# Performance work log

Measured on AMD Instinct MI355X. Metric: run time of the kernel, lower is better.

The kernel has to match this reference:

```python
import jax, jax.numpy as jnp
import numpy as np

B, L, H, U = 4, 4096, 1024, 1024


def setup_inputs() -> dict:
    key = jax.random.key(0)
    k0, k1, k2, k3 = jax.random.split(key, 4)
    inputs = jax.random.normal(k0, (B, L, H), dtype=jnp.float32)
    # linear layer params (torch default init scale ~ 1/sqrt(fan_in))
    W_rkv = jax.random.normal(k1, (H, 3 * U), dtype=jnp.float32) / np.sqrt(H)
    b_rkv = jnp.zeros((3 * U,), dtype=jnp.float32)
    W_o = jax.random.normal(k2, (U, H), dtype=jnp.float32) / np.sqrt(U)
    b_o = jnp.zeros((H,), dtype=jnp.float32)
    # nu_log init exactly as in the torch module
    r_min, r_max = 0.9, 0.999
    u = jax.random.uniform(k3, (U,), dtype=jnp.float32)
    nu_log = jnp.log(-0.5 * jnp.log(u * (r_max ** 2 - r_min ** 2) + r_min ** 2))
    gamma_log = jnp.zeros((U,), dtype=jnp.float32)
    return {"inputs": inputs, "W_rkv": W_rkv, "b_rkv": b_rkv,
            "W_o": W_o, "b_o": b_o, "nu_log": nu_log, "gamma_log": gamma_log}


def reference(inputs, W_rkv, b_rkv, W_o, b_o, nu_log, gamma_log):
    # projections
    rkv = jnp.einsum('blh,hu->blu', inputs, W_rkv) + b_rkv  # [B,L,3U]
    r, k, v = jnp.split(rkv, 3, axis=-1)
    r = jax.nn.sigmoid(r)
    k = jnp.exp(k)
    kv = k * v
    u = jnp.concatenate([kv, k], axis=-1)                   # [B,L,2U]
    nu = jnp.exp(jnp.concatenate([nu_log, nu_log]))         # [2U]
    gamma = jnp.exp(nu_log + gamma_log) - 1.0               # [U]
    lam = jnp.exp(-nu)                                      # per-channel decay
    # The torch log-depth doubling scan computes the linear recurrence
    # y_t = lam * y_{t-1} + u_t (y_0 = u_0). Use an associative scan over L.
    a = jnp.broadcast_to(lam, u.shape)

    def combine(c1, c2):
        a1, x1 = c1
        a2, x2 = c2
        return (a1 * a2, x1 * a2 + x2)

    _, y = jax.lax.associative_scan(combine, (a, u), axis=1)  # [B,L,2U]
    u1, u2 = jnp.split(y, 2, axis=-1)
    x = (u1 + gamma * kv) / (u2 + gamma * k + 1e-6) * r       # [B,L,U]
    return jnp.einsum('blu,uh->blh', x, W_o) + b_o
```

## Files before the change

### kernel.cpp

```cpp
#include <hip/hip_runtime.h>
#include <hip/hip_bf16.h>
#include <cstdint>
#include <cstddef>

constexpr int NB = 4;
constexpr int NL = 4096;
constexpr int NH = 1024;
constexpr int NU = 1024;
constexpr int NM = NB * NL;
constexpr int NCHUNK = 32;
constexpr int CLEN = NL / NCHUNK;

typedef __bf16 bf16x8 __attribute__((ext_vector_type(8)));
typedef __bf16 bf16x4 __attribute__((ext_vector_type(4)));
typedef float  f32x4  __attribute__((ext_vector_type(4)));

__global__ __launch_bounds__(256) void cast_f32_to_bf16(
    const float* __restrict__ in, __bf16* __restrict__ out, int n4) {
  int stride = gridDim.x * 256;
  for (int i = blockIdx.x * 256 + threadIdx.x; i < n4; i += stride) {
    const float4 v = reinterpret_cast<const float4*>(in)[i];
    bf16x4 o;
    o[0] = (__bf16)v.x; o[1] = (__bf16)v.y; o[2] = (__bf16)v.z; o[3] = (__bf16)v.w;
    reinterpret_cast<bf16x4*>(out)[i] = o;
  }
}

__global__ __launch_bounds__(256) void transpose_cast(
    const float* __restrict__ W, __bf16* __restrict__ Wt, int K, int N) {
  __shared__ float tile[32][33];
  int tx = threadIdx.x, ty = threadIdx.y;
  int n0 = blockIdx.x * 32, k0 = blockIdx.y * 32;
  #pragma unroll
  for (int i = 0; i < 32; i += 8)
    tile[ty + i][tx] = W[(size_t)(k0 + ty + i) * N + n0 + tx];
  __syncthreads();
  #pragma unroll
  for (int i = 0; i < 32; i += 8)
    Wt[(size_t)(n0 + ty + i) * K + k0 + tx] = (__bf16)tile[tx][ty + i];
}

constexpr int GBM = 128, GBN = 128, GBK = 64;

template<int EPI>
__global__ __launch_bounds__(256) void gemm_bf16(
    const __bf16* __restrict__ A, const __bf16* __restrict__ Bt,
    int M, int N, int K,
    const float* __restrict__ bias,
    float* __restrict__ out_r, float* __restrict__ out_k, float* __restrict__ out_v,
    float* __restrict__ out_f32) {
  __shared__ __attribute__((aligned(16))) __bf16 lA[GBM * GBK];
  __shared__ __attribute__((aligned(16))) __bf16 lB[GBN * GBK];

  const int tid = threadIdx.x;
  const int lane = tid & 63;
  const int w = tid >> 6;
  const int ntn = N / GBN;
  const int nwg = gridDim.x;
  const int bid = blockIdx.x;
  const int cpx = nwg >> 3;
  const int swz = (bid & 7) * cpx + (bid >> 3);
  const int mt = swz / ntn, nt = swz % ntn;
  const size_t m0 = (size_t)mt * GBM;
  const size_t n0 = (size_t)nt * GBN;

  const int wm = w >> 1, wn = w & 1;

  f32x4 acc[4][4];
  #pragma unroll
  for (int i = 0; i < 4; ++i)
    #pragma unroll
    for (int j = 0; j < 4; ++j) acc[i][j] = (f32x4)0.f;

  const int KT = K / GBK;
  for (int kt = 0; kt < KT; ++kt) {
    #pragma unroll
    for (int i = 0; i < 4; ++i) {
      int chunk = w * 4 + i;
      int off = chunk * 1024 + lane * 16;
      int row = off >> 7;
      int colb = off & 127;
      const __bf16* ga = A + (m0 + row) * K + kt * GBK + (colb >> 1);
      __builtin_amdgcn_global_load_lds(
          (const __attribute__((address_space(1))) unsigned int*)ga,
          (__attribute__((address_space(3))) unsigned int*)((char*)lA + chunk * 1024),
          16, 0, 0);
      const __bf16* gb = Bt + (n0 + row) * K + kt * GBK + (colb >> 1);
      __builtin_amdgcn_global_load_lds(
          (const __attribute__((address_space(1))) unsigned int*)gb,
          (__attribute__((address_space(3))) unsigned int*)((char*)lB + chunk * 1024),
          16, 0, 0);
    }
    __syncthreads();
    #pragma unroll
    for (int kk = 0; kk < GBK; kk += 32) {
      bf16x8 av[4], bv[4];
      #pragma unroll
      for (int f = 0; f < 4; ++f)
        av[f] = *(const bf16x8*)&lA[(wm * 64 + f * 16 + (lane & 15)) * GBK + kk + (lane >> 4) * 8];
      #pragma unroll
      for (int f = 0; f < 4; ++f)
        bv[f] = *(const bf16x8*)&lB[(wn * 64 + f * 16 + (lane & 15)) * GBK + kk + (lane >> 4) * 8];
      #pragma unroll
      for (int i = 0; i < 4; ++i)
        #pragma unroll
        for (int j = 0; j < 4; ++j)
          acc[i][j] = __builtin_amdgcn_mfma_f32_16x16x32_bf16(av[i], bv[j], acc[i][j], 0, 0, 0);
    }
    __syncthreads();
  }

  #pragma unroll
  for (int i = 0; i < 4; ++i) {
    #pragma unroll
    for (int j = 0; j < 4; ++j) {
      #pragma unroll
      for (int r = 0; r < 4; ++r) {
        int row = (int)m0 + wm * 64 + i * 16 + (lane >> 4) * 4 + r;
        int col = (int)n0 + wn * 64 + j * 16 + (lane & 15);
        float val = acc[i][j][r] + bias[col];
        if constexpr (EPI == 0) {
          int reg = col >> 10;
          int u = col & 1023;
          size_t idx = (size_t)row * NU + u;
          if (reg == 0)      out_r[idx] = 1.f / (1.f + __expf(-val));
          else if (reg == 1) out_k[idx] = __expf(val);
          else               out_v[idx] = val;
        } else {
          out_f32[(size_t)row * N + col] = val;
        }
      }
    }
  }
}

__global__ __launch_bounds__(256) void scan_pass1(
    const float* __restrict__ kbuf, const float* __restrict__ vbuf,
    const float* __restrict__ nu_log,
    float* __restrict__ S1, float* __restrict__ S2) {
  int u = blockIdx.x * 256 + threadIdx.x;
  int c = blockIdx.y;
  int b = blockIdx.z;
  float lam = __expf(-__expf(nu_log[u]));
  size_t base = ((size_t)b * NL + (size_t)c * CLEN) * NU + u;
  float y1 = 0.f, y2 = 0.f;
  #pragma unroll 4
  for (int t = 0; t < CLEN; ++t) {
    float kk = kbuf[base + (size_t)t * NU];
    float vv = vbuf[base + (size_t)t * NU];
    y1 = fmaf(lam, y1, kk * vv);
    y2 = fmaf(lam, y2, kk);
  }
  size_t si = ((size_t)b * NCHUNK + c) * NU + u;
  S1[si] = y1;
  S2[si] = y2;
}

__global__ __launch_bounds__(256) void scan_combine(
    const float* __restrict__ S1, const float* __restrict__ S2,
    const float* __restrict__ nu_log,
    float* __restrict__ C1, float* __restrict__ C2) {
  int u = blockIdx.x * 256 + threadIdx.x;
  int b = blockIdx.y;
  float lamCL = __expf(-__expf(nu_log[u]) * (float)CLEN);
  float y1 = 0.f, y2 = 0.f;
  for (int c = 0; c < NCHUNK; ++c) {
    size_t si = ((size_t)b * NCHUNK + c) * NU + u;
    C1[si] = y1;
    C2[si] = y2;
    y1 = fmaf(lamCL, y1, S1[si]);
    y2 = fmaf(lamCL, y2, S2[si]);
  }
}

__global__ __launch_bounds__(256) void scan_pass2(
    const float* __restrict__ kbuf, const float* __restrict__ vbuf,
    const float* __restrict__ rbuf,
    const float* __restrict__ C1, const float* __restrict__ C2,
    const float* __restrict__ nu_log, const float* __restrict__ gamma_log,
    __bf16* __restrict__ xbuf) {
  int u = blockIdx.x * 256 + threadIdx.x;
  int c = blockIdx.y;
  int b = blockIdx.z;
  float lam = __expf(-__expf(nu_log[u]));
  float gamma = __expf(nu_log[u] + gamma_log[u]) - 1.f;
  size_t si = ((size_t)b * NCHUNK + c) * NU + u;
  float y1 = C1[si], y2 = C2[si];
  size_t base = ((size_t)b * NL + (size_t)c * CLEN) * NU + u;
  #pragma unroll 4
  for (int t = 0; t < CLEN; ++t) {
    size_t idx = base + (size_t)t * NU;
    float kk = kbuf[idx];
    float vv = vbuf[idx];
    float rr = rbuf[idx];
    float kv = kk * vv;
    y1 = fmaf(lam, y1, kv);
    y2 = fmaf(lam, y2, kk);
    float x = (y1 + gamma * kv) / (y2 + gamma * kk + 1e-6f) * rr;
    xbuf[idx] = (__bf16)x;
  }
}

extern "C" void kernel_launch(void* const* d_in, const int* in_sizes, int n_in,
                              void* d_out, int out_size, void* d_ws, size_t ws_size,
                              hipStream_t stream) {
  const float* inputs    = (const float*)d_in[0];
  const float* W_rkv     = (const float*)d_in[1];
  const float* b_rkv     = (const float*)d_in[2];
  const float* W_o       = (const float*)d_in[3];
  const float* b_o       = (const float*)d_in[4];
  const float* nu_log    = (const float*)d_in[5];
  const float* gamma_log = (const float*)d_in[6];
  float* out = (float*)d_out;

  char* ws = (char*)d_ws;
  size_t off = 0;
  __bf16* Abuf  = (__bf16*)(ws + off); off += (size_t)NM * NH * 2;
  __bf16* WrkvT = (__bf16*)(ws + off); off += (size_t)3 * NU * NH * 2;
  __bf16* WoT   = (__bf16*)(ws + off); off += (size_t)NH * NU * 2;
  float*  rbuf  = (float*)(ws + off);  off += (size_t)NM * NU * 4;
  float*  kbuf  = (float*)(ws + off);  off += (size_t)NM * NU * 4;
  float*  vbuf  = (float*)(ws + off);  off += (size_t)NM * NU * 4;
  float*  S1    = (float*)(ws + off);  off += (size_t)NB * NCHUNK * NU * 4;
  float*  S2    = (float*)(ws + off);  off += (size_t)NB * NCHUNK * NU * 4;
  float*  C1    = (float*)(ws + off);  off += (size_t)NB * NCHUNK * NU * 4;
  float*  C2    = (float*)(ws + off);  off += (size_t)NB * NCHUNK * NU * 4;
  __bf16* xbuf  = Abuf;

  cast_f32_to_bf16<<<2048, 256, 0, stream>>>(inputs, Abuf, (NM * NH) / 4);

  transpose_cast<<<dim3(3 * NU / 32, NH / 32), dim3(32, 8), 0, stream>>>(W_rkv, WrkvT, NH, 3 * NU);
  transpose_cast<<<dim3(NH / 32, NU / 32), dim3(32, 8), 0, stream>>>(W_o, WoT, NU, NH);

  gemm_bf16<0><<<(NM / GBM) * (3 * NU / GBN), 256, 0, stream>>>(
      Abuf, WrkvT, NM, 3 * NU, NH, b_rkv, rbuf, kbuf, vbuf, nullptr);

  scan_pass1<<<dim3(NU / 256, NCHUNK, NB), 256, 0, stream>>>(kbuf, vbuf, nu_log, S1, S2);
  scan_combine<<<dim3(NU / 256, NB), 256, 0, stream>>>(S1, S2, nu_log, C1, C2);
  scan_pass2<<<dim3(NU / 256, NCHUNK, NB), 256, 0, stream>>>(
      kbuf, vbuf, rbuf, C1, C2, nu_log, gamma_log, xbuf);

  gemm_bf16<1><<<(NM / GBM) * (NH / GBN), 256, 0, stream>>>(
      xbuf, WoT, NM, NH, NU, b_o, nullptr, nullptr, nullptr, out);
}
```

Before: 420.6 us.

## Replace 128x128 GEMM with 256x256 double-buffered, swizzled, phased MFMA GEMM

```diff
diff --git a/kernel.cpp b/kernel.cpp
--- a/kernel.cpp
+++ b/kernel.cpp
@@ -40,88 +40,151 @@
     Wt[(size_t)(n0 + ty + i) * K + k0 + tx] = (__bf16)tile[tx][ty + i];
 }
 
-constexpr int GBM = 128, GBN = 128, GBK = 64;
+
+#define SBAR0 __builtin_amdgcn_sched_barrier(0)
 
 template<int EPI>
-__global__ __launch_bounds__(256) void gemm_bf16(
+__global__ __launch_bounds__(512, 2) void gemm256(
     const __bf16* __restrict__ A, const __bf16* __restrict__ Bt,
     int M, int N, int K,
     const float* __restrict__ bias,
     float* __restrict__ out_r, float* __restrict__ out_k, float* __restrict__ out_v,
     float* __restrict__ out_f32) {
-  __shared__ __attribute__((aligned(16))) __bf16 lA[GBM * GBK];
-  __shared__ __attribute__((aligned(16))) __bf16 lB[GBN * GBK];
+  __shared__ __attribute__((aligned(16))) __bf16 sA[2][256 * 64];
+  __shared__ __attribute__((aligned(16))) __bf16 sB[2][256 * 64];
 
   const int tid = threadIdx.x;
   const int lane = tid & 63;
   const int w = tid >> 6;
-  const int ntn = N / GBN;
+  const int wm = w >> 2, wn = w & 3;
+
+  const int ntn = N >> 8;
   const int nwg = gridDim.x;
   const int bid = blockIdx.x;
   const int cpx = nwg >> 3;
   const int swz = (bid & 7) * cpx + (bid >> 3);
   const int mt = swz / ntn, nt = swz % ntn;
-  const size_t m0 = (size_t)mt * GBM;
-  const size_t n0 = (size_t)nt * GBN;
-
-  const int wm = w >> 1, wn = w & 1;
-
-  f32x4 acc[4][4];
-  #pragma unroll
-  for (int i = 0; i < 4; ++i)
+  const long m0 = (long)mt * 256;
+  const long n0 = (long)nt * 256;
+  const int KT = K >> 6;
+
+  const int srow = lane >> 3;
+  const int scol = ((lane & 7) ^ srow) << 4;
+
+  auto stageA = [&](int bi, int qm, int t) {
+    if (t >= KT) return;
+    #pragma unroll
+    for (int j = 0; j < 2; ++j) {
+      int u = w * 2 + j;
+      int row0 = (u < 8) ? (qm * 64 + u * 8) : (128 + qm * 64 + (u - 8) * 8);
+      const char* src = (const char*)A + ((m0 + row0 + srow) * (long)K + (long)t * 64) * 2 + scol;
+      __builtin_amdgcn_global_load_lds(
+          (const __attribute__((address_space(1))) unsigned int*)src,
+          (__attribute__((address_space(3))) unsigned int*)((char*)&sA[bi][0] + row0 * 128),
+          16, 0, 0);
+    }
+  };
+  auto stageB = [&](int bi, int qn, int t) {
+    if (t >= KT) return;
+    #pragma unroll
+    for (int j = 0; j < 2; ++j) {
+      int u = w * 2 + j;
+      int row0 = (u >> 2) * 64 + qn * 32 + (u & 3) * 8;
+      const char* src = (const char*)Bt + ((n0 + row0 + srow) * (long)K + (long)t * 64) * 2 + scol;
+      __builtin_amdgcn_global_load_lds(
+          (const __attribute__((address_space(1))) unsigned int*)src,
+          (__attribute__((address_space(3))) unsigned int*)((char*)&sB[bi][0] + row0 * 128),
+          16, 0, 0);
+    }
+  };
+
+  f32x4 acc[8][4];
+  #pragma unroll
+  for (int i = 0; i < 8; ++i)
     #pragma unroll
     for (int j = 0; j < 4; ++j) acc[i][j] = (f32x4)0.f;
 
-  const int KT = K / GBK;
-  for (int kt = 0; kt < KT; ++kt) {
+#define PHASE(QM, QN, STAGE_STMT)                                              \
+  do {                                                                         \
+    const char* sAb = (const char*)&sA[bi][0];                                 \
+    const char* sBb = (const char*)&sB[bi][0];                                 \
+    bf16x8 av[4][2], bv[2][2];                                                 \
+    _Pragma("unroll")                                                          \
+    for (int f = 0; f < 4; ++f) {                                              \
+      _Pragma("unroll")                                                        \
+      for (int ks = 0; ks < 2; ++ks) {                                         \
+        int r = wm * 128 + ((QM) * 4 + f) * 16 + (lane & 15);                  \
+        int c = ks * 64 + (lane & 48);                                         \
+        av[f][ks] = *(const bf16x8*)(sAb + r * 128 + (c ^ ((r & 7) << 4)));    \
+      }                                                                        \
+    }                                                                          \
+    _Pragma("unroll")                                                          \
+    for (int g = 0; g < 2; ++g) {                                              \
+      _Pragma("unroll")                                                        \
+      for (int ks = 0; ks < 2; ++ks) {                                         \
+        int r = wn * 64 + ((QN) * 2 + g) * 16 + (lane & 15);                   \
+        int c = ks * 64 + (lane & 48);                                         \
+        bv[g][ks] = *(const bf16x8*)(sBb + r * 128 + (c ^ ((r & 7) << 4)));    \
+      }                                                                        \
+    }                                                                          \
+    STAGE_STMT;                                                                \
+    SBAR0;                                                                     \
+    __builtin_amdgcn_s_barrier();                                              \
+    SBAR0;                                                                     \
+    __builtin_amdgcn_s_setprio(1);                                             \
+    _Pragma("unroll")                                                          \
+    for (int f = 0; f < 4; ++f) {                                              \
+      _Pragma("unroll")                                                        \
+      for (int g = 0; g < 2; ++g) {                                            \
+        acc[(QM) * 4 + f][(QN) * 2 + g] = __builtin_amdgcn_mfma_f32_16x16x32_bf16( \
+            av[f][0], bv[g][0], acc[(QM) * 4 + f][(QN) * 2 + g], 0, 0, 0);     \
+        acc[(QM) * 4 + f][(QN) * 2 + g] = __builtin_amdgcn_mfma_f32_16x16x32_bf16( \
+            av[f][1], bv[g][1], acc[(QM) * 4 + f][(QN) * 2 + g], 0, 0, 0);     \
+      }                                                                        \
+    }                                                                          \
+    __builtin_amdgcn_s_setprio(0);                                             \
+    SBAR0;                                                                     \
+  } while (0)
+
+#define EBAR { __builtin_amdgcn_s_barrier(); SBAR0; }
+
+  stageA(0, 0, 0); stageB(0, 0, 0); stageA(0, 1, 0); stageB(0, 1, 0);
+  stageA(1, 0, 1); stageB(1, 0, 1);
+  SBAR0;
+  asm volatile("s_waitcnt vmcnt(4)" ::: "memory");
+  EBAR;
+
+  for (int t = 0; t < KT; ++t) {
+    const int bi = t & 1;
+    PHASE(0, 0, stageB(bi ^ 1, 1, t + 1)); EBAR;
+    PHASE(1, 0, stageA(bi ^ 1, 1, t + 1)); EBAR;
+    PHASE(0, 1, stageB(bi, 0, t + 2));     EBAR;
+    PHASE(1, 1, stageA(bi, 0, t + 2));
+    SBAR0;
+    if (t < KT - 2) { asm volatile("s_waitcnt vmcnt(4)" ::: "memory"); }
+    else            { asm volatile("s_waitcnt vmcnt(0)" ::: "memory"); }
+    EBAR;
+  }
+#undef PHASE
+#undef EBAR
+
+  float bs[4];
+  #pragma unroll
+  for (int fn = 0; fn < 4; ++fn)
+    bs[fn] = bias[n0 + wn * 64 + fn * 16 + (lane & 15)];
+
+  #pragma unroll
+  for (int fm = 0; fm < 8; ++fm) {
     #pragma unroll
-    for (int i = 0; i < 4; ++i) {
-      int chunk = w * 4 + i;
-      int off = chunk * 1024 + lane * 16;
-      int row = off >> 7;
-      int colb = off & 127;
-      const __bf16* ga = A + (m0 + row) * K + kt * GBK + (colb >> 1);
-      __builtin_amdgcn_global_load_lds(
-          (const __attribute__((address_space(1))) unsigned int*)ga,
-          (__attribute__((address_space(3))) unsigned int*)((char*)lA + chunk * 1024),
-          16, 0, 0);
-      const __bf16* gb = Bt + (n0 + row) * K + kt * GBK + (colb >> 1);
-      __builtin_amdgcn_global_load_lds(
-          (const __attribute__((address_space(1))) unsigned int*)gb,
-          (__attribute__((address_space(3))) unsigned int*)((char*)lB + chunk * 1024),
-          16, 0, 0);
-    }
-    __syncthreads();
-    #pragma unroll
-    for (int kk = 0; kk < GBK; kk += 32) {
-      bf16x8 av[4], bv[4];
+    for (int fn = 0; fn < 4; ++fn) {
       #pragma unroll
-      for (int f = 0; f < 4; ++f)
-        av[f] = *(const bf16x8*)&lA[(wm * 64 + f * 16 + (lane & 15)) * GBK + kk + (lane >> 4) * 8];
-      #pragma unroll
-      for (int f = 0; f < 4; ++f)
-        bv[f] = *(const bf16x8*)&lB[(wn * 64 + f * 16 + (lane & 15)) * GBK + kk + (lane >> 4) * 8];
-      #pragma unroll
-      for (int i = 0; i < 4; ++i)
-        #pragma unroll
-        for (int j = 0; j < 4; ++j)
-          acc[i][j] = __builtin_amdgcn_mfma_f32_16x16x32_bf16(av[i], bv[j], acc[i][j], 0, 0, 0);
-    }
-    __syncthreads();
-  }
-
-  #pragma unroll
-  for (int i = 0; i < 4; ++i) {
-    #pragma unroll
-    for (int j = 0; j < 4; ++j) {
-      #pragma unroll
-      for (int r = 0; r < 4; ++r) {
-        int row = (int)m0 + wm * 64 + i * 16 + (lane >> 4) * 4 + r;
-        int col = (int)n0 + wn * 64 + j * 16 + (lane & 15);
-        float val = acc[i][j][r] + bias[col];
+      for (int rr = 0; rr < 4; ++rr) {
+        long row = m0 + wm * 128 + fm * 16 + (lane >> 4) * 4 + rr;
+        long col = n0 + wn * 64 + fn * 16 + (lane & 15);
+        float val = acc[fm][fn][rr] + bs[fn];
         if constexpr (EPI == 0) {
-          int reg = col >> 10;
-          int u = col & 1023;
+          int reg = (int)(col >> 10);
+          int u = (int)(col & 1023);
           size_t idx = (size_t)row * NU + u;
           if (reg == 0)      out_r[idx] = 1.f / (1.f + __expf(-val));
           else if (reg == 1) out_k[idx] = __expf(val);
@@ -232,7 +295,7 @@
   transpose_cast<<<dim3(3 * NU / 32, NH / 32), dim3(32, 8), 0, stream>>>(W_rkv, WrkvT, NH, 3 * NU);
   transpose_cast<<<dim3(NH / 32, NU / 32), dim3(32, 8), 0, stream>>>(W_o, WoT, NU, NH);
 
-  gemm_bf16<0><<<(NM / GBM) * (3 * NU / GBN), 256, 0, stream>>>(
+  gemm256<0><<<(NM / 256) * (3 * NU / 256), 512, 0, stream>>>(
       Abuf, WrkvT, NM, 3 * NU, NH, b_rkv, rbuf, kbuf, vbuf, nullptr);
 
   scan_pass1<<<dim3(NU / 256, NCHUNK, NB), 256, 0, stream>>>(kbuf, vbuf, nu_log, S1, S2);
@@ -240,6 +303,6 @@
   scan_pass2<<<dim3(NU / 256, NCHUNK, NB), 256, 0, stream>>>(
       kbuf, vbuf, rbuf, C1, C2, nu_log, gamma_log, xbuf);
 
-  gemm_bf16<1><<<(NM / GBM) * (NH / GBN), 256, 0, stream>>>(
+  gemm256<1><<<(NM / 256) * (NH / 256), 512, 0, stream>>>(
       xbuf, WoT, NM, NH, NU, b_o, nullptr, nullptr, nullptr, out);
 }
```

Measured after the change: 368.1 us. 1.14x faster.
